# Performance work log

Hardware: AMD Instinct MI355X
Metric: run time of the kernel (lower is better)

The kernel has to match this reference:

```python
import jax, jax.numpy as jnp
import numpy as np

B, SM, SI, D, H, FF = 4, 1024, 4096, 256, 8, 1024
EPS = 1e-6

def _ln(x, g, b):
    m = jnp.mean(x, axis=-1, keepdims=True)
    v = jnp.mean(jnp.square(x - m), axis=-1, keepdims=True)
    return (x - m) * jax.lax.rsqrt(v + EPS) * g + b

def setup_inputs() -> dict:
    key = jax.random.key(0)
    ks = jax.random.split(key, 12)
    s = 0.02
    return {
        "state_seq": jax.random.normal(ks[0], (B, SM, D), jnp.float32),
        "input_seq": jax.random.normal(ks[1], (B, SI, D), jnp.float32),
        "Wk": jax.random.normal(ks[2], (D, D), jnp.float32) * s,
        "bk": jnp.zeros((D,), jnp.float32),
        "Wv": jax.random.normal(ks[3], (D, D), jnp.float32) * s,
        "bv": jnp.zeros((D,), jnp.float32),
        "Wq": jax.random.normal(ks[4], (H, D, D), jnp.float32) * s,
        "bq": jnp.zeros((H, D), jnp.float32),
        "Wo": jax.random.normal(ks[5], (H * D, D), jnp.float32) * s,
        "bo": jnp.zeros((D,), jnp.float32),
        "ln1_g": jnp.ones((D,), jnp.float32),
        "ln1_b": jnp.zeros((D,), jnp.float32),
        "W_in": jax.random.normal(ks[6], (D, FF), jnp.float32) * s,
        "b_in": jnp.zeros((FF,), jnp.float32),
        "Wg_nl": jax.random.normal(ks[7], (FF, FF), jnp.float32) * s,
        "bg_nl": jnp.zeros((FF,), jnp.float32),
        "Wg_l": jax.random.normal(ks[8], (FF, FF), jnp.float32) * s,
        "bg_l": jnp.zeros((FF,), jnp.float32),
        "Wg_o": jax.random.normal(ks[9], (FF, D), jnp.float32) * s,
        "bg_o": jnp.zeros((D,), jnp.float32),
        "ln2_g": jnp.ones((D,), jnp.float32),
        "ln2_b": jnp.zeros((D,), jnp.float32),
    }

def reference(state_seq, input_seq, Wk, bk, Wv, bv, Wq, bq, Wo, bo,
              ln1_g, ln1_b, W_in, b_in, Wg_nl, bg_nl, Wg_l, bg_l, Wg_o, bg_o,
              ln2_g, ln2_b):
    # shared key/value projections (multi-query: one K/V, many Q)
    ik = input_seq @ Wk + bk            # [B,SI,D]
    mk = state_seq @ Wk + bk            # [B,SM,D]
    iv = input_seq @ Wv + bv            # [B,SI,D]
    mv = state_seq @ Wv + bv            # [B,SM,D]
    # per-head queries from memory cells, stacked over H
    q = jnp.einsum('bmd,hde->hbme', state_seq, Wq) + bq[:, None, None, :]  # [H,B,SM,D]
    input_score = jnp.einsum('hbme,bse->hbms', q, ik)                      # [H,B,SM,SI]
    self_score = jnp.sum(q * mk[None], axis=-1, keepdims=True)             # [H,B,SM,1]
    score = jnp.concatenate([self_score, input_score], axis=-1)
    score = score / jnp.sqrt(jnp.asarray(D, score.dtype))
    attn = jax.nn.softmax(score, axis=-1)                                  # [H,B,SM,1+SI]
    val = jnp.einsum('hbms,bse->hbme', attn[..., 1:], iv) + attn[..., 0:1] * mv[None]
    concat = jnp.transpose(val, (1, 2, 0, 3)).reshape(val.shape[1], val.shape[2], -1)  # [B,SM,H*D]
    attn_out = concat @ Wo + bo
    x = _ln(attn_out + state_seq, ln1_g, ln1_b)
    h = jax.nn.relu(x @ W_in + b_in)                                       # [B,SM,FF]
    g = jax.nn.relu(h @ Wg_nl + bg_nl) * (h @ Wg_l + bg_l)
    ff = g @ Wg_o + bg_o
    return _ln(ff + x, ln2_g, ln2_b)
```

## Files before the change

### kernel.cpp

```cpp
#include <hip/hip_runtime.h>
#include <hip/hip_bf16.h>

typedef __bf16 bfx8 __attribute__((ext_vector_type(8)));
typedef __bf16 bfx4 __attribute__((ext_vector_type(4)));
typedef float  f32x4 __attribute__((ext_vector_type(4)));
typedef float  f32x16 __attribute__((ext_vector_type(16)));

#define MFMA16(a,b,c) __builtin_amdgcn_mfma_f32_16x16x32_bf16((a),(b),(c),0,0,0)
#define MFMA32(a,b,c) __builtin_amdgcn_mfma_f32_32x32x16_bf16((a),(b),(c),0,0,0)


__device__ __forceinline__ void tile_tr(const float* __restrict__ src, __bf16* __restrict__ dst,
                                        int R, int C, int tile, float (*lt)[65]) {
  int tpr = C >> 6;
  int tr = tile / tpr, tc = tile % tpr;
  int c  = threadIdx.x & 63;
  int r0 = (threadIdx.x >> 6) << 4;
  const float* sp = src + (long)(tr * 64 + r0) * C + tc * 64 + c;
#pragma unroll
  for (int i = 0; i < 16; i++) lt[r0 + i][c] = sp[(long)i * C];
  __syncthreads();
  __bf16* dp = dst + (long)(tc * 64 + r0) * R + tr * 64 + c;
#pragma unroll
  for (int i = 0; i < 16; i++) dp[(long)i * R] = (__bf16)lt[c][r0 + i];
}

__global__ void trans_attn_t(const float* __restrict__ Wk, const float* __restrict__ Wv,
                             const float* __restrict__ Wq, const float* __restrict__ Wo,
                             __bf16* __restrict__ wkvqt, __bf16* __restrict__ wot) {
  __shared__ float lt[64][65];
  int t = blockIdx.x;
  if (t < 16)       tile_tr(Wk, wkvqt, 256, 256, t, lt);
  else if (t < 32)  tile_tr(Wv, wkvqt + 65536, 256, 256, t - 16, lt);
  else if (t < 160) {
    int e = t - 32, m = e >> 4;
    tile_tr(Wq + (long)m * 65536, wkvqt + 131072 + (long)m * 65536, 256, 256, e & 15, lt);
  } else            tile_tr(Wo, wot, 2048, 256, t - 160, lt);
}

__global__ void trans_ffn_t(const float* __restrict__ W_in, const float* __restrict__ Wg_nl,
                            const float* __restrict__ Wg_l, const float* __restrict__ Wg_o,
                            __bf16* __restrict__ dst) {
  __shared__ float lt[64][65];
  int t = blockIdx.x;
  if (t < 64)       tile_tr(W_in, dst, 256, 1024, t, lt);
  else if (t < 320) tile_tr(Wg_nl, dst + 262144, 1024, 1024, t - 64, lt);
  else if (t < 576) tile_tr(Wg_l, dst + 1310720, 1024, 1024, t - 320, lt);
  else              tile_tr(Wg_o, dst + 2359296, 1024, 256, t - 576, lt);
}

__device__ __forceinline__
void gemm_body(const __bf16* __restrict__ Xb, const float* __restrict__ Xf,
               const __bf16* __restrict__ Wt,
               const float* __restrict__ b1, const float* __restrict__ b2,
               const float* __restrict__ b3,
               __bf16* __restrict__ C, __bf16* __restrict__ C2, __bf16* __restrict__ C3,
               float* __restrict__ Cf,
               int M, int N, int Kfull, int kspan, int xmode, int mode, int act,
               int bx, int by, int bz, __bf16* xs, __bf16* wsm) {
  const int tid  = threadIdx.x;
  const int lane = tid & 63;
  const int w    = tid >> 6;
  const int l15  = lane & 15;
  const int quad = lane >> 4;
  const int wm   = (w >> 1) * 64;
  const int wn   = (w & 1) * 64;
  const int m0   = bx * 128;
  const int n0   = by * 128;
  const int k0   = (mode == 7) ? bz * kspan : 0;

  f32x4 acc[4][4];
#pragma unroll
  for (int i = 0; i < 4; i++)
#pragma unroll
    for (int j = 0; j < 4; j++) acc[i][j] = (f32x4){0.f, 0.f, 0.f, 0.f};

  for (int kk = k0; kk < k0 + kspan; kk += 64) {
    __syncthreads();
#pragma unroll
    for (int rep = 0; rep < 4; rep++) {
      int idx = rep * 256 + tid;
      int row = idx >> 3;
      int g   = idx & 7;
      if (xmode == 1) {
        const float* p = Xf + (long)(m0 + row) * Kfull + kk + g * 8;
        f32x4 a0 = *(const f32x4*)p;
        f32x4 a1 = *(const f32x4*)(p + 4);
        bfx8 v;
#pragma unroll
        for (int j = 0; j < 4; j++) { v[j] = (__bf16)a0[j]; v[4 + j] = (__bf16)a1[j]; }
        *(bfx8*)&xs[row * 72 + g * 8] = v;
      } else if (xmode == 2) {
        const __bf16* p = Xb + (long)(m0 + row) * 2048 + kk + g * 8;
        bfx8 a = *(const bfx8*)p;
        bfx8 bb = *(const bfx8*)(p + 1024);
        bfx8 v;
#pragma unroll
        for (int j = 0; j < 8; j++) v[j] = (__bf16)((float)a[j] * (float)bb[j]);
        *(bfx8*)&xs[row * 72 + g * 8] = v;
      } else {
        *(bfx8*)&xs[row * 72 + g * 8] = *(const bfx8*)(Xb + (long)(m0 + row) * Kfull + kk + g * 8);
      }
      *(bfx8*)&wsm[row * 72 + g * 8] = *(const bfx8*)(Wt + (long)(n0 + row) * Kfull + kk + g * 8);
    }
    __syncthreads();
#pragma unroll
    for (int ks = 0; ks < 2; ks++) {
      bfx8 af[4], bf_[4];
#pragma unroll
      for (int i = 0; i < 4; i++) af[i]  = *(const bfx8*)&xs[(wm + 16 * i + l15) * 72 + ks * 32 + quad * 8];
#pragma unroll
      for (int j = 0; j < 4; j++) bf_[j] = *(const bfx8*)&wsm[(wn + 16 * j + l15) * 72 + ks * 32 + quad * 8];
#pragma unroll
      for (int i = 0; i < 4; i++)
#pragma unroll
        for (int j = 0; j < 4; j++) acc[i][j] = MFMA16(af[i], bf_[j], acc[i][j]);
    }
  }

#pragma unroll
  for (int j = 0; j < 4; j++) {
    int n = n0 + wn + 16 * j + l15;
    float bv;
    if (mode == 4)      bv = (n < 256) ? b1[n] : b2[n - 256];
    else if (mode == 5) bv = (n < 256) ? b1[n] : (n < 512) ? b2[n - 256] : b3[n - 512];
    else if (mode == 6) bv = (n < 1024) ? b1[n] : b2[n - 1024];
    else if (mode == 7) bv = (bz == 0) ? b1[n] : 0.f;
    else                bv = b1[n];
#pragma unroll
    for (int i = 0; i < 4; i++) {
#pragma unroll
      for (int r = 0; r < 4; r++) {
        int m = m0 + wm + 16 * i + quad * 4 + r;
        float v = acc[i][j][r] + bv;
        if (mode == 6) { if (n < 1024) v = fmaxf(v, 0.f); }
        else if (act == 1) v = fmaxf(v, 0.f);
        if (mode == 4) {
          if (n < 256) C[(long)m * 256 + n] = (__bf16)v;
          else {
            int bb_ = m >> 12, si = m & 4095;
            C2[((long)(bb_ * 128 + (si >> 5)) * 256 + (n - 256)) * 32 + (si & 31)] = (__bf16)v;
          }
        } else if (mode == 5) {
          if (n < 256)      C[(long)m * 256 + n] = (__bf16)v;
          else if (n < 512) C2[(long)m * 256 + (n - 256)] = (__bf16)v;
          else {
            int nn = n - 512, hh = nn >> 8, dd = nn & 255;
            C3[(long)hh * 1048576 + (long)m * 256 + dd] = (__bf16)v;
          }
        } else if (mode == 7) {
          Cf[(long)bz * M * N + (long)m * N + n] = v;
        } else {
          C[(long)m * N + n] = (__bf16)v;
        }
      }
    }
  }
}

__global__ __launch_bounds__(256)
void gemm_bt(const __bf16* Xb, const float* Xf, const __bf16* Wt,
             const float* b1, const float* b2, const float* b3,
             __bf16* C, __bf16* C2, __bf16* C3, float* Cf,
             int M, int N, int Kfull, int kspan, int xmode, int mode, int act) {
  __shared__ __bf16 xs[128 * 72];
  __shared__ __bf16 wsm[128 * 72];
  gemm_body(Xb, Xf, Wt, b1, b2, b3, C, C2, C3, Cf, M, N, Kfull, kspan, xmode, mode, act,
            blockIdx.x, blockIdx.y, blockIdx.z, xs, wsm);
}

__global__ __launch_bounds__(256)
void proj2(const float* input, const float* state, const __bf16* Wkvqt,
           const float* bk, const float* bv, const float* bq,
           __bf16* ik, __bf16* ivT, __bf16* mk, __bf16* mv, __bf16* qbuf) {
  __shared__ __bf16 xs[128 * 72];
  __shared__ __bf16 wsm[128 * 72];
  int bid = blockIdx.x;
  if (bid < 512) {
    gemm_body(nullptr, input, Wkvqt, bk, bv, nullptr, ik, ivT, nullptr, nullptr,
              16384, 512, 256, 256, 1, 4, 0, bid & 127, bid >> 7, 0, xs, wsm);
  } else {
    int b2 = bid - 512;
    gemm_body(nullptr, state, Wkvqt, bk, bv, bq, mk, mv, qbuf, nullptr,
              4096, 2560, 256, 256, 1, 5, 0, b2 & 31, b2 >> 5, 0, xs, wsm);
  }
}

__global__ __launch_bounds__(256)
void attn_kernel(const __bf16* __restrict__ qb,
                 const __bf16* __restrict__ ik,
                 const __bf16* __restrict__ ivT,
                 const __bf16* __restrict__ mk,
                 const __bf16* __restrict__ mv,
                 __bf16* __restrict__ concat) {
  __shared__ __bf16 lk[2][32][264];
  __shared__ __bf16 lvt[2][256][40];
  __shared__ __bf16 lp[128][40];

  const int tid  = threadIdx.x;
  const int lane = tid & 63;
  const int w    = tid >> 6;
  const int l31  = lane & 31;
  const int h    = lane >> 5;

  const int m0 = blockIdx.x * 128;
  const int b  = blockIdx.y;
  const int hh = blockIdx.z;
  const int mw = m0 + w * 32;

  const long qbase  = ((long)hh * 4096 + b * 1024 + mw) * 256;
  const long kvbase = (long)b * 4096 * 256;
  const long vtbase = (long)b * 128 * 8192;
  const long mbase  = ((long)b * 1024 + mw) * 256;

  bfx8 qf[16];
  {
    const __bf16* qrow = qb + qbase + (long)l31 * 256 + h * 8;
#pragma unroll
    for (int kt = 0; kt < 16; kt++) qf[kt] = *(const bfx8*)(qrow + kt * 16);
  }

  float ps_l;
  {
    const __bf16* krow = mk + mbase + (long)l31 * 256 + h * 8;
    float s = 0.f;
#pragma unroll
    for (int kt = 0; kt < 16; kt++) {
      bfx8 kv = *(const bfx8*)(krow + kt * 16);
#pragma unroll
      for (int j = 0; j < 8; j++) s += (float)qf[kt][j] * (float)kv[j];
    }
    s += __shfl_xor(s, 32);
    ps_l = __expf(fminf(s * 0.0625f, 30.f));
  }

  bfx8 onesf;
#pragma unroll
  for (int j = 0; j < 8; j++) onesf[j] = (__bf16)1.0f;

  f32x16 oacc[8];
  f32x16 dacc;
#pragma unroll
  for (int i = 0; i < 16; i++) dacc[i] = 0.f;
#pragma unroll
  for (int dt = 0; dt < 8; dt++)
#pragma unroll
    for (int i = 0; i < 16; i++) oacc[dt][i] = 0.f;

#pragma unroll
  for (int rep = 0; rep < 4; rep++) {
    int idx = rep * 256 + tid;
    *(bfx8*)&lk[0][idx >> 5][(idx & 31) * 8] =
        *(const bfx8*)(ik + kvbase + (long)(idx >> 5) * 256 + (idx & 31) * 8);
    *(bfx8*)&lvt[0][idx >> 2][(idx & 3) * 8] = *(const bfx8*)(ivT + vtbase + (long)idx * 8);
  }
  __syncthreads();

  for (int sc = 0; sc < 128; sc++) {
    const int cur = sc & 1;
    bfx8 kreg[4], vreg[4];
    if (sc < 127) {
      const long kb = kvbase + (long)(sc + 1) * 8192;
      const long vb = vtbase + (long)(sc + 1) * 8192;
#pragma unroll
      for (int rep = 0; rep < 4; rep++) {
        int idx = rep * 256 + tid;
        kreg[rep] = *(const bfx8*)(ik + kb + (long)(idx >> 5) * 256 + (idx & 31) * 8);
        vreg[rep] = *(const bfx8*)(ivT + vb + (long)idx * 8);
      }
    }

    f32x16 sacc;
#pragma unroll
    for (int i = 0; i < 16; i++) sacc[i] = 0.f;
#pragma unroll
    for (int kt = 0; kt < 16; kt++) {
      bfx8 kf = *(const bfx8*)&lk[cur][l31][kt * 16 + h * 8];
      sacc = MFMA32(qf[kt], kf, sacc);
    }

#pragma unroll
    for (int r = 0; r < 16; r++) {
      int row = (r & 3) + 8 * (r >> 2) + 4 * h;
      lp[w * 32 + row][l31] = (__bf16)__expf(fminf(sacc[r] * 0.0625f, 30.f));
    }

    bfx8 pf0 = *(const bfx8*)&lp[w * 32 + l31][h * 8];
    bfx8 pf1 = *(const bfx8*)&lp[w * 32 + l31][16 + h * 8];
    dacc = MFMA32(pf0, onesf, dacc);
    dacc = MFMA32(pf1, onesf, dacc);
#pragma unroll
    for (int dt = 0; dt < 8; dt++) {
      bfx8 vf0 = *(const bfx8*)&lvt[cur][dt * 32 + l31][h * 8];
      bfx8 vf1 = *(const bfx8*)&lvt[cur][dt * 32 + l31][16 + h * 8];
      oacc[dt] = MFMA32(pf0, vf0, oacc[dt]);
      oacc[dt] = MFMA32(pf1, vf1, oacc[dt]);
    }

    if (sc < 127) {
#pragma unroll
      for (int rep = 0; rep < 4; rep++) {
        int idx = rep * 256 + tid;
        *(bfx8*)&lk[cur ^ 1][idx >> 5][(idx & 31) * 8] = kreg[rep];
        *(bfx8*)&lvt[cur ^ 1][idx >> 2][(idx & 3) * 8] = vreg[rep];
      }
    }
    __syncthreads();
  }

#pragma unroll
  for (int r = 0; r < 16; r++) {
    int row = (r & 3) + 8 * (r >> 2) + 4 * h;
    float ps = __shfl(ps_l, row);
    float dinv = 1.f / (dacc[r] + ps);
    const __bf16* mvrow = mv + mbase + (long)row * 256;
    __bf16* crow = concat + ((long)(b * 1024 + mw + row)) * 2048 + hh * 256;
#pragma unroll
    for (int dt = 0; dt < 8; dt++) {
      int d = dt * 32 + l31;
      crow[d] = (__bf16)((oacc[dt][r] + ps * (float)mvrow[d]) * dinv);
    }
  }
}

__global__ __launch_bounds__(256)
void ln4_kernel(const float* __restrict__ parts, const float* __restrict__ res,
                const float* __restrict__ g, const float* __restrict__ beta,
                __bf16* __restrict__ outb, float* __restrict__ outf) {
  int row  = blockIdx.x * 4 + (threadIdx.x >> 6);
  int lane = threadIdx.x & 63;
  const float* p = parts + (long)row * 256 + lane * 4;
  f32x4 a0 = *(const f32x4*)p;
  f32x4 a1 = *(const f32x4*)(p + 1048576);
  f32x4 a2 = *(const f32x4*)(p + 2097152);
  f32x4 a3 = *(const f32x4*)(p + 3145728);
  f32x4 rv = *(const f32x4*)(res + (long)row * 256 + lane * 4);
  float v[4], s1 = 0.f, s2 = 0.f;
#pragma unroll
  for (int i = 0; i < 4; i++) {
    v[i] = a0[i] + a1[i] + a2[i] + a3[i] + rv[i];
    s1 += v[i];
    s2 += v[i] * v[i];
  }
#pragma unroll
  for (int off = 32; off >= 1; off >>= 1) {
    s1 += __shfl_xor(s1, off);
    s2 += __shfl_xor(s2, off);
  }
  float mean = s1 * (1.f / 256.f);
  float var  = fmaxf(s2 * (1.f / 256.f) - mean * mean, 0.f);
  float rstd = rsqrtf(var + 1e-6f);
#pragma unroll
  for (int i = 0; i < 4; i++) {
    int c = lane * 4 + i;
    float o = (v[i] - mean) * rstd * g[c] + beta[c];
    if (outb) outb[(long)row * 256 + c] = (__bf16)o;
    if (outf) outf[(long)row * 256 + c] = o;
  }
}

extern "C" void kernel_launch(void* const* d_in, const int* in_sizes, int n_in,
                              void* d_out, int out_size, void* d_ws, size_t ws_size,
                              hipStream_t stream) {
  const float* state  = (const float*)d_in[0];
  const float* input  = (const float*)d_in[1];
  const float* Wk     = (const float*)d_in[2];
  const float* bk     = (const float*)d_in[3];
  const float* Wv     = (const float*)d_in[4];
  const float* bv     = (const float*)d_in[5];
  const float* Wq     = (const float*)d_in[6];
  const float* bq     = (const float*)d_in[7];
  const float* Wo     = (const float*)d_in[8];
  const float* bo     = (const float*)d_in[9];
  const float* ln1g   = (const float*)d_in[10];
  const float* ln1b   = (const float*)d_in[11];
  const float* W_in   = (const float*)d_in[12];
  const float* b_in   = (const float*)d_in[13];
  const float* Wg_nl  = (const float*)d_in[14];
  const float* bg_nl  = (const float*)d_in[15];
  const float* Wg_l   = (const float*)d_in[16];
  const float* bg_l   = (const float*)d_in[17];
  const float* Wg_o   = (const float*)d_in[18];
  const float* bg_o   = (const float*)d_in[19];
  const float* ln2g   = (const float*)d_in[20];
  const float* ln2b   = (const float*)d_in[21];
  float* out = (float*)d_out;

  const size_t needed_elems = 28442624;
  if (ws_size < needed_elems * sizeof(__bf16)) return;

  __bf16* ws = (__bf16*)d_ws;
  size_t off = 0;
  auto alloc = [&](size_t n) { __bf16* p = ws + off; off += n; return p; };
  __bf16* Wkvqt  = alloc(655360);
  __bf16* Wot    = alloc(524288);
  __bf16* ik     = alloc(4194304);
  __bf16* ivT    = alloc(4194304);
  __bf16* mk     = alloc(1048576);
  __bf16* mv     = alloc(1048576);
  __bf16* qbuf   = alloc(8388608);
  __bf16* concat = alloc(8388608);
  float*  wo_parts = (float*)qbuf;
  __bf16* x      = mv;
  __bf16* hbuf   = ik;
  __bf16* t12    = qbuf;
  float*  ff_parts = (float*)ik;
  __bf16* Wffn   = concat;
  float*  xf     = (float*)(concat + 3670016);

  dim3 blk(256);

  trans_attn_t<<<dim3(288), blk, 0, stream>>>(Wk, Wv, Wq, Wo, Wkvqt, Wot);

  proj2<<<dim3(1152), blk, 0, stream>>>(input, state, Wkvqt, bk, bv, bq,
                                        ik, ivT, mk, mv, qbuf);

  attn_kernel<<<dim3(8, 4, 8), blk, 0, stream>>>(qbuf, ik, ivT, mk, mv, concat);

  gemm_bt<<<dim3(32, 2, 4), blk, 0, stream>>>(concat, nullptr, Wot, bo, nullptr, nullptr,
                                              nullptr, nullptr, nullptr, wo_parts,
                                              4096, 256, 2048, 512, 0, 7, 0);
  ln4_kernel<<<dim3(1024), blk, 0, stream>>>(wo_parts, state, ln1g, ln1b, x, xf);

  trans_ffn_t<<<dim3(640), blk, 0, stream>>>(W_in, Wg_nl, Wg_l, Wg_o, Wffn);

  gemm_bt<<<dim3(32, 8), blk, 0, stream>>>(x, nullptr, Wffn, b_in, nullptr, nullptr,
                                           hbuf, nullptr, nullptr, nullptr,
                                           4096, 1024, 256, 256, 0, 0, 1);
  gemm_bt<<<dim3(32, 16), blk, 0, stream>>>(hbuf, nullptr, Wffn + 262144, bg_nl, bg_l, nullptr,
                                            t12, nullptr, nullptr, nullptr,
                                            4096, 2048, 1024, 1024, 0, 6, 0);
  gemm_bt<<<dim3(32, 2, 4), blk, 0, stream>>>(t12, nullptr, Wffn + 2359296, bg_o, nullptr, nullptr,
                                              nullptr, nullptr, nullptr, ff_parts,
                                              4096, 256, 1024, 256, 2, 7, 0);
  ln4_kernel<<<dim3(1024), blk, 0, stream>>>(ff_parts, xf, ln2g, ln2b, nullptr, out);
}
```

Baseline: 489.2 us.

## Software-pipeline attention: overlap QK^T of next chunk with PV, keep P in registers

Restructures the attention inner loop so the score MFMAs for chunk i+1 are interleaved with the PV MFMAs for chunk i. V uses a triple-buffered LDS slot and K stays double-buffered. Scores are computed transposed (K as the A operand) so P can be converted in registers with v_cvt_pk_bf16_f32 and v_permlane32_swap instead of going through an LDS scratch tile. The row-sum denominator MFMAs against a ones vector are replaced by scalar accumulation plus a cross-half shuffle. The aim is to remove the LDS round trip and the extra MFMAs, and to hide exp latency behind matrix work, at the cost of higher register pressure and more complex buffer indexing.

```diff
diff --git a/kernel.cpp b/kernel.cpp
--- a/kernel.cpp
+++ b/kernel.cpp
@@ -9,6 +9,24 @@
 #define MFMA16(a,b,c) __builtin_amdgcn_mfma_f32_16x16x32_bf16((a),(b),(c),0,0,0)
 #define MFMA32(a,b,c) __builtin_amdgcn_mfma_f32_32x32x16_bf16((a),(b),(c),0,0,0)
 
+
+__device__ __forceinline__ unsigned cvtpk_bf16(float lo, float hi) {
+  unsigned d;
+  asm("v_cvt_pk_bf16_f32 %0, %1, %2" : "=v"(d) : "v"(lo), "v"(hi));
+  return d;
+}
+
+__device__ __forceinline__ bfx8 packswap(const float* p) {
+  unsigned a = cvtpk_bf16(p[0], p[1]);
+  unsigned b = cvtpk_bf16(p[2], p[3]);
+  unsigned c = cvtpk_bf16(p[4], p[5]);
+  unsigned d = cvtpk_bf16(p[6], p[7]);
+  asm("v_permlane32_swap_b32 %0, %1" : "+v"(a), "+v"(c));
+  asm("v_permlane32_swap_b32 %0, %1" : "+v"(b), "+v"(d));
+  union { unsigned u[4]; bfx8 v; } uu;
+  uu.u[0] = a; uu.u[1] = b; uu.u[2] = c; uu.u[3] = d;
+  return uu.v;
+}
 
 __device__ __forceinline__ void tile_tr(const float* __restrict__ src, __bf16* __restrict__ dst,
                                         int R, int C, int tile, float (*lt)[65]) {
@@ -145,8 +163,8 @@
           if (n < 256)      C[(long)m * 256 + n] = (__bf16)v;
           else if (n < 512) C2[(long)m * 256 + (n - 256)] = (__bf16)v;
           else {
-            int nn = n - 512, hh = nn >> 8, dd = nn & 255;
-            C3[(long)hh * 1048576 + (long)m * 256 + dd] = (__bf16)v;
+            int nn = n - 512, hhh = nn >> 8, dd = nn & 255;
+            C3[(long)hhh * 1048576 + (long)m * 256 + dd] = (__bf16)v;
           }
         } else if (mode == 7) {
           Cf[(long)bz * M * N + (long)m * N + n] = v;
@@ -194,8 +212,7 @@
                  const __bf16* __restrict__ mv,
                  __bf16* __restrict__ concat) {
   __shared__ __bf16 lk[2][32][264];
-  __shared__ __bf16 lvt[2][256][40];
-  __shared__ __bf16 lp[128][40];
+  __shared__ __bf16 lvt[3][256][40];
 
   const int tid  = threadIdx.x;
   const int lane = tid & 63;
@@ -234,85 +251,109 @@
     ps_l = __expf(fminf(s * 0.0625f, 30.f));
   }
 
-  bfx8 onesf;
-#pragma unroll
-  for (int j = 0; j < 8; j++) onesf[j] = (__bf16)1.0f;
-
   f32x16 oacc[8];
-  f32x16 dacc;
-#pragma unroll
-  for (int i = 0; i < 16; i++) dacc[i] = 0.f;
 #pragma unroll
   for (int dt = 0; dt < 8; dt++)
 #pragma unroll
     for (int i = 0; i < 16; i++) oacc[dt][i] = 0.f;
-
-#pragma unroll
-  for (int rep = 0; rep < 4; rep++) {
-    int idx = rep * 256 + tid;
-    *(bfx8*)&lk[0][idx >> 5][(idx & 31) * 8] =
-        *(const bfx8*)(ik + kvbase + (long)(idx >> 5) * 256 + (idx & 31) * 8);
-    *(bfx8*)&lvt[0][idx >> 2][(idx & 3) * 8] = *(const bfx8*)(ivT + vtbase + (long)idx * 8);
+  float den_l = 0.f;
+  bfx8 pf0c, pf1c;
+
+  f32x16 zz;
+#pragma unroll
+  for (int i = 0; i < 16; i++) zz[i] = 0.f;
+
+  auto sload = [&](int c, bfx8* kreg, bfx8* vreg) {
+    const long kb = kvbase + (long)c * 8192;
+    const long vb = vtbase + (long)c * 8192;
+#pragma unroll
+    for (int rep = 0; rep < 4; rep++) {
+      int idx = rep * 256 + tid;
+      kreg[rep] = *(const bfx8*)(ik + kb + (long)(idx >> 5) * 256 + (idx & 31) * 8);
+      vreg[rep] = *(const bfx8*)(ivT + vb + (long)idx * 8);
+    }
+  };
+  auto sstore = [&](int kslot, int vslot, const bfx8* kreg, const bfx8* vreg) {
+#pragma unroll
+    for (int rep = 0; rep < 4; rep++) {
+      int idx = rep * 256 + tid;
+      *(bfx8*)&lk[kslot][idx >> 5][(idx & 31) * 8] = kreg[rep];
+      *(bfx8*)&lvt[vslot][idx >> 2][(idx & 3) * 8] = vreg[rep];
+    }
+  };
+
+  auto chunkMFMA = [&](int vslot, int kslot, bool doS, bool doPV, f32x16* sa) {
+#pragma unroll
+    for (int t = 0; t < 8; t++) {
+      bfx8 vf0, vf1, kf0, kf1;
+      if (doPV) {
+        vf0 = *(const bfx8*)&lvt[vslot][t * 32 + l31][h * 8];
+        vf1 = *(const bfx8*)&lvt[vslot][t * 32 + l31][16 + h * 8];
+      }
+      if (doS) {
+        kf0 = *(const bfx8*)&lk[kslot][l31][(2 * t) * 16 + h * 8];
+        kf1 = *(const bfx8*)&lk[kslot][l31][(2 * t + 1) * 16 + h * 8];
+      }
+      if (doPV) oacc[t] = MFMA32(pf0c, vf0, oacc[t]);
+      if (doS) {
+        if (t < 2) sa[2 * t] = MFMA32(kf0, qf[2 * t], zz);
+        else       sa[(2 * t) & 3] = MFMA32(kf0, qf[2 * t], sa[(2 * t) & 3]);
+      }
+      if (doPV) oacc[t] = MFMA32(pf1c, vf1, oacc[t]);
+      if (doS) {
+        if (t < 2) sa[2 * t + 1] = MFMA32(kf1, qf[2 * t + 1], zz);
+        else       sa[(2 * t + 1) & 3] = MFMA32(kf1, qf[2 * t + 1], sa[(2 * t + 1) & 3]);
+      }
+    }
+  };
+
+  auto finishP = [&](const f32x16* sa) {
+    float p[16];
+#pragma unroll
+    for (int r = 0; r < 16; r++) {
+      float s = (sa[0][r] + sa[1][r]) + (sa[2][r] + sa[3][r]);
+      p[r] = __expf(fminf(s * 0.0625f, 30.f));
+      den_l += p[r];
+    }
+    pf0c = packswap(p);
+    pf1c = packswap(p + 8);
+  };
+
+  {
+    bfx8 kreg[4], vreg[4];
+    sload(0, kreg, vreg);
+    sstore(0, 0, kreg, vreg);
+    sload(1, kreg, vreg);
+    sstore(1, 1, kreg, vreg);
   }
   __syncthreads();
 
-  for (int sc = 0; sc < 128; sc++) {
-    const int cur = sc & 1;
+  f32x16 sa[4];
+  chunkMFMA(0, 0, true, false, sa);
+  finishP(sa);
+  __syncthreads();
+
+  int vcur = 0, vnst = 2;
+  for (int i = 0; i < 126; i++) {
     bfx8 kreg[4], vreg[4];
-    if (sc < 127) {
-      const long kb = kvbase + (long)(sc + 1) * 8192;
-      const long vb = vtbase + (long)(sc + 1) * 8192;
-#pragma unroll
-      for (int rep = 0; rep < 4; rep++) {
-        int idx = rep * 256 + tid;
-        kreg[rep] = *(const bfx8*)(ik + kb + (long)(idx >> 5) * 256 + (idx & 31) * 8);
-        vreg[rep] = *(const bfx8*)(ivT + vb + (long)idx * 8);
-      }
-    }
-
-    f32x16 sacc;
-#pragma unroll
-    for (int i = 0; i < 16; i++) sacc[i] = 0.f;
-#pragma unroll
-    for (int kt = 0; kt < 16; kt++) {
-      bfx8 kf = *(const bfx8*)&lk[cur][l31][kt * 16 + h * 8];
-      sacc = MFMA32(qf[kt], kf, sacc);
-    }
-
-#pragma unroll
-    for (int r = 0; r < 16; r++) {
-      int row = (r & 3) + 8 * (r >> 2) + 4 * h;
-      lp[w * 32 + row][l31] = (__bf16)__expf(fminf(sacc[r] * 0.0625f, 30.f));
-    }
-
-    bfx8 pf0 = *(const bfx8*)&lp[w * 32 + l31][h * 8];
-    bfx8 pf1 = *(const bfx8*)&lp[w * 32 + l31][16 + h * 8];
-    dacc = MFMA32(pf0, onesf, dacc);
-    dacc = MFMA32(pf1, onesf, dacc);
-#pragma unroll
-    for (int dt = 0; dt < 8; dt++) {
-      bfx8 vf0 = *(const bfx8*)&lvt[cur][dt * 32 + l31][h * 8];
-      bfx8 vf1 = *(const bfx8*)&lvt[cur][dt * 32 + l31][16 + h * 8];
-      oacc[dt] = MFMA32(pf0, vf0, oacc[dt]);
-      oacc[dt] = MFMA32(pf1, vf1, oacc[dt]);
-    }
-
-    if (sc < 127) {
-#pragma unroll
-      for (int rep = 0; rep < 4; rep++) {
-        int idx = rep * 256 + tid;
-        *(bfx8*)&lk[cur ^ 1][idx >> 5][(idx & 31) * 8] = kreg[rep];
-        *(bfx8*)&lvt[cur ^ 1][idx >> 2][(idx & 3) * 8] = vreg[rep];
-      }
-    }
+    sload(i + 2, kreg, vreg);
+    chunkMFMA(vcur, (i + 1) & 1, true, true, sa);
+    sstore(i & 1, vnst, kreg, vreg);
+    finishP(sa);
     __syncthreads();
-  }
-
+    vcur = (vcur == 2) ? 0 : vcur + 1;
+    vnst = (vnst == 2) ? 0 : vnst + 1;
+  }
+  chunkMFMA(0, 1, true, true, sa);
+  finishP(sa);
+  chunkMFMA(1, 0, false, true, sa);
+
+  float tot = den_l + __shfl_xor(den_l, 32) + ps_l;
 #pragma unroll
   for (int r = 0; r < 16; r++) {
     int row = (r & 3) + 8 * (r >> 2) + 4 * h;
-    float ps = __shfl(ps_l, row);
-    float dinv = 1.f / (dacc[r] + ps);
+    float ps   = __shfl(ps_l, row);
+    float dinv = 1.f / __shfl(tot, row);
     const __bf16* mvrow = mv + mbase + (long)row * 256;
     __bf16* crow = concat + ((long)(b * 1024 + mw + row)) * 2048 + hh * 256;
 #pragma unroll
```

Result: faster. 451.6 us (-7.7%).
